# Kernel optimization log

Measured on AMD Instinct MI355X. Metric: run time of the kernel, lower is better.

Reference implementation:

```python
import jax, jax.numpy as jnp
import numpy as np

# SMPL kinematic tree parents (parent index < child index, so a forward loop is valid)
PARENTS = np.array([-1, 0, 0, 0, 1, 2, 3, 4, 5, 6, 7, 8, 9, 9, 9, 12, 13, 14, 16, 17, 18, 19, 20, 21], dtype=np.int32)

B = 131072      # batch
J = 24          # num_joints
D = 6           # dim_per_joint
F = 13 + D      # per-joint MLP width = 19


def setup_inputs() -> dict:
    key = jax.random.key(0)
    ks = jax.random.split(key, 8)
    rots = jax.random.normal(ks[0], (B, J, 9), dtype=jnp.float32)
    Jtrs = jax.random.normal(ks[1], (B, J, 3), dtype=jnp.float32)
    # layer_0: Linear(9*J + 3*J -> D), torch convention W:[out,in]
    W0 = jax.random.normal(ks[2], (D, 12 * J), dtype=jnp.float32) * 0.05
    b0 = jnp.zeros((D,), dtype=jnp.float32)
    # per-joint MLPs, stacked: Linear(F->F), ReLU, Linear(F->D)
    W1 = jax.random.normal(ks[3], (J, F, F), dtype=jnp.float32) * 0.2
    b1 = jnp.zeros((J, F), dtype=jnp.float32)
    W2 = jax.random.normal(ks[4], (J, D, F), dtype=jnp.float32) * 0.2
    b2 = jnp.zeros((J, D), dtype=jnp.float32)
    return {"rots": rots, "Jtrs": Jtrs, "W0": W0, "b0": b0,
            "W1": W1, "b1": b1, "W2": W2, "b2": b2}


def reference(rots, Jtrs, W0, b0, W1, b1, W2, b2):
    bsz = rots.shape[0]
    # global feature: concat flattened rots and Jtrs -> Linear -> [B, D]
    gfeat = jnp.concatenate([rots.reshape(bsz, -1), Jtrs.reshape(bsz, -1)], axis=-1)
    gfeat = gfeat @ W0.T + b0
    out = [None] * J
    for j in range(J):  # fixed small structural loop over kinematic tree
        rot = rots[:, j, :]   # [B, 9]
        jtr = Jtrs[:, j, :]   # [B, 3]
        p = int(PARENTS[j])
        if p == -1:
            bone_l = jnp.linalg.norm(jtr, axis=-1, keepdims=True)  # [B, 1]
            feat = gfeat
        else:
            bone_l = jnp.linalg.norm(jtr - Jtrs[:, p, :], axis=-1, keepdims=True)
            feat = out[p]
        x = jnp.concatenate([rot, jtr, bone_l, feat], axis=-1)     # [B, 19]
        h = jax.nn.relu(x @ W1[j].T + b1[j])
        out[j] = h @ W2[j].T + b2[j]                               # [B, 6]
    return jnp.concatenate(out, axis=-1)  # [B, 144]
```

## Files before the change

kernel.cpp:

```cpp
#include <hip/hip_runtime.h>
#include <math.h>

#define BLK 256

constexpr int PAR_CT[24] = {-1,0,0,0,1,2,3,4,5,6,7,8,9,9,9,12,13,14,16,17,18,19,20,21};

template<int M>
__device__ __forceinline__ float4 bcast_f4(const float4 (&s)[14]) {
    constexpr int lane = M & 3, reg = M >> 2;
    float4 v = s[reg], r;
    r.x = __shfl(v.x, lane, 4);
    r.y = __shfl(v.y, lane, 4);
    r.z = __shfl(v.z, lane, 4);
    r.w = __shfl(v.w, lane, 4);
    return r;
}

template<int E>
__device__ __forceinline__ float bcast_jt(const float4 (&s)[5]) {
    constexpr int m = E >> 2, lane = m & 3, reg = m >> 2, c = E & 3;
    float4 v = s[reg];
    float x = (c == 0) ? v.x : (c == 1) ? v.y : (c == 2) ? v.z : v.w;
    return __shfl(x, lane, 4);
}

template<int J>
__device__ __forceinline__ void joint_step(const float4 (&rot_s)[14],
                                           const float4 (&jt_s)[5],
                                           const float* __restrict__ W1s,
                                           const float* __restrict__ W2s,
                                           const float* __restrict__ b2,
                                           const float (&gf)[6],
                                           float (&o)[24][6],
                                           float* __restrict__ orow,
                                           int l)
{
    constexpr int P = PAR_CT[J];

    const float jx = bcast_jt<3*J+0>(jt_s);
    const float jy = bcast_jt<3*J+1>(jt_s);
    const float jz = bcast_jt<3*J+2>(jt_s);
    float dx, dy, dz;
    if constexpr (P < 0) { dx = jx; dy = jy; dz = jz; }
    else {
        const float px = bcast_jt<3*P+0>(jt_s);
        const float py = bcast_jt<3*P+1>(jt_s);
        const float pz = bcast_jt<3*P+2>(jt_s);
        dx = jx - px; dy = jy - py; dz = jz - pz;
    }
    const float bl = sqrtf(dx*dx + dy*dy + dz*dz);

    constexpr int w0  = (9*J) / 4;
    constexpr int off = (9*J) % 4;
    float4 A = bcast_f4<w0  >(rot_s);
    float4 B = bcast_f4<w0+1>(rot_s);
    float4 C = bcast_f4<w0+2>(rot_s);
    float rv[12] = {A.x,A.y,A.z,A.w, B.x,B.y,B.z,B.w, C.x,C.y,C.z,C.w};

    float f0,f1,f2,f3,f4v,f5;
    if constexpr (P < 0) { f0=gf[0]; f1=gf[1]; f2=gf[2]; f3=gf[3]; f4v=gf[4]; f5=gf[5]; }
    else { f0=o[P][0]; f1=o[P][1]; f2=o[P][2]; f3=o[P][3]; f4v=o[P][4]; f5=o[P][5]; }

    float h[5];
    #pragma unroll
    for (int u = 0; u < 5; ++u) {
        const int r = l + 4*u;
        if (r < 19) {
            const float* w = W1s + J*380 + r*20;
            float4 wa = *(const float4*)(w);
            float4 wb = *(const float4*)(w + 4);
            float4 wc = *(const float4*)(w + 8);
            float4 wd = *(const float4*)(w + 12);
            float4 we = *(const float4*)(w + 16);
            float acc = we.w;
            acc = fmaf(rv[off+0], wa.x, acc);
            acc = fmaf(rv[off+1], wa.y, acc);
            acc = fmaf(rv[off+2], wa.z, acc);
            acc = fmaf(rv[off+3], wa.w, acc);
            acc = fmaf(rv[off+4], wb.x, acc);
            acc = fmaf(rv[off+5], wb.y, acc);
            acc = fmaf(rv[off+6], wb.z, acc);
            acc = fmaf(rv[off+7], wb.w, acc);
            acc = fmaf(rv[off+8], wc.x, acc);
            acc = fmaf(jx, wc.y, acc);
            acc = fmaf(jy, wc.z, acc);
            acc = fmaf(jz, wc.w, acc);
            acc = fmaf(bl, wd.x, acc);
            acc = fmaf(f0, wd.y, acc);
            acc = fmaf(f1, wd.z, acc);
            acc = fmaf(f2, wd.w, acc);
            acc = fmaf(f3, we.x, acc);
            acc = fmaf(f4v, we.y, acc);
            acc = fmaf(f5, we.z, acc);
            h[u] = fmaxf(acc, 0.0f);
        }
    }

    float od[6] = {0,0,0,0,0,0};
    #pragma unroll
    for (int u = 0; u < 5; ++u) {
        const int r = l + 4*u;
        if (r < 19) {
            const float* w = W2s + J*152 + r*8;
            float4 wa = *(const float4*)(w);
            float4 wb = *(const float4*)(w + 4);
            od[0] = fmaf(h[u], wa.x, od[0]);
            od[1] = fmaf(h[u], wa.y, od[1]);
            od[2] = fmaf(h[u], wa.z, od[2]);
            od[3] = fmaf(h[u], wa.w, od[3]);
            od[4] = fmaf(h[u], wb.x, od[4]);
            od[5] = fmaf(h[u], wb.y, od[5]);
        }
    }

    #pragma unroll
    for (int d = 0; d < 6; ++d) {
        od[d] += __shfl_xor(od[d], 1, 4);
        od[d] += __shfl_xor(od[d], 2, 4);
        od[d] += b2[J*6 + d];
        o[J][d] = od[d];
    }

    if constexpr (J & 1) {
        if (l < 3) {
            float4 v;
            if (l == 0)      { v.x = o[J-1][0]; v.y = o[J-1][1]; v.z = o[J-1][2]; v.w = o[J-1][3]; }
            else if (l == 1) { v.x = o[J-1][4]; v.y = o[J-1][5]; v.z = o[J][0];   v.w = o[J][1];   }
            else             { v.x = o[J][2];   v.y = o[J][3];   v.z = o[J][4];   v.w = o[J][5];   }
            *reinterpret_cast<float4*>(orow + (J-1)*6 + 4*l) = v;
        }
    }
}

template<int J>
__device__ __forceinline__ void run_chain(const float4 (&rot_s)[14],
                                          const float4 (&jt_s)[5],
                                          const float* __restrict__ W1s,
                                          const float* __restrict__ W2s,
                                          const float* __restrict__ b2,
                                          const float (&gf)[6],
                                          float (&o)[24][6],
                                          float* __restrict__ orow,
                                          int l)
{
    if constexpr (J < 24) {
        joint_step<J>(rot_s, jt_s, W1s, W2s, b2, gf, o, orow, l);
        run_chain<J+1>(rot_s, jt_s, W1s, W2s, b2, gf, o, orow, l);
    }
}

__global__ __launch_bounds__(BLK, 3)
void pose_kernel(const float* __restrict__ rots,
                 const float* __restrict__ jtrs,
                 const float* __restrict__ W0,
                 const float* __restrict__ b0,
                 const float* __restrict__ W1,
                 const float* __restrict__ b1,
                 const float* __restrict__ W2,
                 const float* __restrict__ b2,
                 float* __restrict__ out,
                 int bsz)
{
    __shared__ __align__(16) float W1s[24*19*20];
    __shared__ __align__(16) float W2s[24*19*8];

    for (int idx = threadIdx.x; idx < 24*19*20; idx += BLK) {
        int j = idx / 380, rem = idx % 380, r = rem / 20, c = rem % 20;
        W1s[idx] = (c < 19) ? W1[(j*19 + r)*19 + c] : b1[j*19 + r];
    }
    for (int idx = threadIdx.x; idx < 24*19*8; idx += BLK) {
        int j = idx / 152, rem = idx % 152, r = rem / 8, d = rem % 8;
        W2s[idx] = (d < 6) ? W2[(j*6 + d)*19 + r] : 0.0f;
    }
    __syncthreads();

    const int t   = blockIdx.x * BLK + threadIdx.x;
    const int row = t >> 2;
    const int l   = t & 3;
    if (row >= bsz) return;

    const float4* rp = reinterpret_cast<const float4*>(rots + (size_t)row * 216);
    const float4* jp = reinterpret_cast<const float4*>(jtrs + (size_t)row * 72);
    float* orow = out + (size_t)row * 144;

    float4 rot_s[14];
    #pragma unroll
    for (int i = 0; i < 13; ++i) rot_s[i] = rp[4*i + l];
    if (l < 2) rot_s[13] = rp[52 + l];

    float4 jt_s[5];
    #pragma unroll
    for (int i = 0; i < 4; ++i) jt_s[i] = jp[4*i + l];
    if (l < 2) jt_s[4] = jp[16 + l];

    float gf[6] = {0,0,0,0,0,0};
    #pragma unroll
    for (int i = 0; i < 13; ++i) {
        const int m = 4*i + l;
        float4 v = rot_s[i];
        #pragma unroll
        for (int d = 0; d < 6; ++d) {
            float4 w = *reinterpret_cast<const float4*>(W0 + d*288 + 4*m);
            gf[d] = fmaf(v.x, w.x, gf[d]);
            gf[d] = fmaf(v.y, w.y, gf[d]);
            gf[d] = fmaf(v.z, w.z, gf[d]);
            gf[d] = fmaf(v.w, w.w, gf[d]);
        }
    }
    if (l < 2) {
        const int m = 52 + l;
        float4 v = rot_s[13];
        #pragma unroll
        for (int d = 0; d < 6; ++d) {
            float4 w = *reinterpret_cast<const float4*>(W0 + d*288 + 4*m);
            gf[d] = fmaf(v.x, w.x, gf[d]);
            gf[d] = fmaf(v.y, w.y, gf[d]);
            gf[d] = fmaf(v.z, w.z, gf[d]);
            gf[d] = fmaf(v.w, w.w, gf[d]);
        }
    }
    #pragma unroll
    for (int i = 0; i < 4; ++i) {
        const int m = 4*i + l;
        float4 v = jt_s[i];
        #pragma unroll
        for (int d = 0; d < 6; ++d) {
            float4 w = *reinterpret_cast<const float4*>(W0 + d*288 + 216 + 4*m);
            gf[d] = fmaf(v.x, w.x, gf[d]);
            gf[d] = fmaf(v.y, w.y, gf[d]);
            gf[d] = fmaf(v.z, w.z, gf[d]);
            gf[d] = fmaf(v.w, w.w, gf[d]);
        }
    }
    if (l < 2) {
        const int m = 16 + l;
        float4 v = jt_s[4];
        #pragma unroll
        for (int d = 0; d < 6; ++d) {
            float4 w = *reinterpret_cast<const float4*>(W0 + d*288 + 216 + 4*m);
            gf[d] = fmaf(v.x, w.x, gf[d]);
            gf[d] = fmaf(v.y, w.y, gf[d]);
            gf[d] = fmaf(v.z, w.z, gf[d]);
            gf[d] = fmaf(v.w, w.w, gf[d]);
        }
    }
    #pragma unroll
    for (int d = 0; d < 6; ++d) {
        gf[d] += __shfl_xor(gf[d], 1, 4);
        gf[d] += __shfl_xor(gf[d], 2, 4);
        gf[d] += b0[d];
    }

    float o[24][6];
    run_chain<0>(rot_s, jt_s, W1s, W2s, b2, gf, o, orow, l);
}

extern "C" void kernel_launch(void* const* d_in, const int* in_sizes, int n_in,
                              void* d_out, int out_size, void* d_ws, size_t ws_size,
                              hipStream_t stream)
{
    const float* rots = (const float*)d_in[0];
    const float* jtrs = (const float*)d_in[1];
    const float* W0   = (const float*)d_in[2];
    const float* b0   = (const float*)d_in[3];
    const float* W1   = (const float*)d_in[4];
    const float* b1   = (const float*)d_in[5];
    const float* W2   = (const float*)d_in[6];
    const float* b2   = (const float*)d_in[7];
    float* out = (float*)d_out;

    int bsz = in_sizes[0] / 216;
    long long threads = (long long)bsz * 4;
    int blocks = (int)((threads + BLK - 1) / BLK);
    hipLaunchKernelGGL(pose_kernel, dim3(blocks), dim3(BLK), 0, stream,
                       rots, jtrs, W0, b0, W1, b1, W2, b2, out, bsz);
}
```

Before: 342.3 us.

## Interleave independent kinematic-tree joints in groups to expose instruction-level parallelism

Replaces the strictly sequential per-joint chain with groups of up to three joints whose parents are already computed, interleaving their layer-1 and layer-2 computations and shuffle reductions. The goal is to hide shuffle and LDS latency along the serial dependency chain by overlapping independent work. This raises register pressure (three sets of rotation, h and od values live at once), which may cause spills under the launch bounds of 3 blocks.

```diff
diff --git a/kernel.cpp b/kernel.cpp
--- a/kernel.cpp
+++ b/kernel.cpp
@@ -24,95 +24,106 @@
     return __shfl(x, lane, 4);
 }
 
-template<int J>
-__device__ __forceinline__ void joint_step(const float4 (&rot_s)[14],
-                                           const float4 (&jt_s)[5],
-                                           const float* __restrict__ W1s,
-                                           const float* __restrict__ W2s,
-                                           const float* __restrict__ b2,
-                                           const float (&gf)[6],
-                                           float (&o)[24][6],
-                                           float* __restrict__ orow,
-                                           int l)
+struct JS {
+    float rv[12];
+    float jx, jy, jz, bl;
+};
+
+template<int J>
+__device__ __forceinline__ void prep(const float4 (&rot_s)[14], const float4 (&jt_s)[5], JS& s)
 {
     constexpr int P = PAR_CT[J];
-
-    const float jx = bcast_jt<3*J+0>(jt_s);
-    const float jy = bcast_jt<3*J+1>(jt_s);
-    const float jz = bcast_jt<3*J+2>(jt_s);
+    s.jx = bcast_jt<3*J+0>(jt_s);
+    s.jy = bcast_jt<3*J+1>(jt_s);
+    s.jz = bcast_jt<3*J+2>(jt_s);
     float dx, dy, dz;
-    if constexpr (P < 0) { dx = jx; dy = jy; dz = jz; }
+    if constexpr (P < 0) { dx = s.jx; dy = s.jy; dz = s.jz; }
     else {
         const float px = bcast_jt<3*P+0>(jt_s);
         const float py = bcast_jt<3*P+1>(jt_s);
         const float pz = bcast_jt<3*P+2>(jt_s);
-        dx = jx - px; dy = jy - py; dz = jz - pz;
-    }
-    const float bl = sqrtf(dx*dx + dy*dy + dz*dz);
-
-    constexpr int w0  = (9*J) / 4;
-    constexpr int off = (9*J) % 4;
+        dx = s.jx - px; dy = s.jy - py; dz = s.jz - pz;
+    }
+    s.bl = sqrtf(dx*dx + dy*dy + dz*dz);
+
+    constexpr int w0 = (9*J) / 4;
     float4 A = bcast_f4<w0  >(rot_s);
     float4 B = bcast_f4<w0+1>(rot_s);
     float4 C = bcast_f4<w0+2>(rot_s);
-    float rv[12] = {A.x,A.y,A.z,A.w, B.x,B.y,B.z,B.w, C.x,C.y,C.z,C.w};
-
-    float f0,f1,f2,f3,f4v,f5;
-    if constexpr (P < 0) { f0=gf[0]; f1=gf[1]; f2=gf[2]; f3=gf[3]; f4v=gf[4]; f5=gf[5]; }
-    else { f0=o[P][0]; f1=o[P][1]; f2=o[P][2]; f3=o[P][3]; f4v=o[P][4]; f5=o[P][5]; }
-
-    float h[5];
-    #pragma unroll
-    for (int u = 0; u < 5; ++u) {
-        const int r = l + 4*u;
-        if (r < 19) {
-            const float* w = W1s + J*380 + r*20;
-            float4 wa = *(const float4*)(w);
-            float4 wb = *(const float4*)(w + 4);
-            float4 wc = *(const float4*)(w + 8);
-            float4 wd = *(const float4*)(w + 12);
-            float4 we = *(const float4*)(w + 16);
-            float acc = we.w;
-            acc = fmaf(rv[off+0], wa.x, acc);
-            acc = fmaf(rv[off+1], wa.y, acc);
-            acc = fmaf(rv[off+2], wa.z, acc);
-            acc = fmaf(rv[off+3], wa.w, acc);
-            acc = fmaf(rv[off+4], wb.x, acc);
-            acc = fmaf(rv[off+5], wb.y, acc);
-            acc = fmaf(rv[off+6], wb.z, acc);
-            acc = fmaf(rv[off+7], wb.w, acc);
-            acc = fmaf(rv[off+8], wc.x, acc);
-            acc = fmaf(jx, wc.y, acc);
-            acc = fmaf(jy, wc.z, acc);
-            acc = fmaf(jz, wc.w, acc);
-            acc = fmaf(bl, wd.x, acc);
-            acc = fmaf(f0, wd.y, acc);
-            acc = fmaf(f1, wd.z, acc);
-            acc = fmaf(f2, wd.w, acc);
-            acc = fmaf(f3, we.x, acc);
-            acc = fmaf(f4v, we.y, acc);
-            acc = fmaf(f5, we.z, acc);
-            h[u] = fmaxf(acc, 0.0f);
-        }
-    }
-
-    float od[6] = {0,0,0,0,0,0};
-    #pragma unroll
-    for (int u = 0; u < 5; ++u) {
-        const int r = l + 4*u;
-        if (r < 19) {
-            const float* w = W2s + J*152 + r*8;
-            float4 wa = *(const float4*)(w);
-            float4 wb = *(const float4*)(w + 4);
-            od[0] = fmaf(h[u], wa.x, od[0]);
-            od[1] = fmaf(h[u], wa.y, od[1]);
-            od[2] = fmaf(h[u], wa.z, od[2]);
-            od[3] = fmaf(h[u], wa.w, od[3]);
-            od[4] = fmaf(h[u], wb.x, od[4]);
-            od[5] = fmaf(h[u], wb.y, od[5]);
-        }
-    }
-
+    s.rv[0]=A.x; s.rv[1]=A.y; s.rv[2]=A.z; s.rv[3]=A.w;
+    s.rv[4]=B.x; s.rv[5]=B.y; s.rv[6]=B.z; s.rv[7]=B.w;
+    s.rv[8]=C.x; s.rv[9]=C.y; s.rv[10]=C.z; s.rv[11]=C.w;
+}
+
+template<int J>
+__device__ __forceinline__ void l1row(const JS& s, const float (&gf)[6], const float (&o)[24][6],
+                                      int u, int l, const float* __restrict__ W1s, float (&h)[5])
+{
+    constexpr int P   = PAR_CT[J];
+    constexpr int off = (9*J) % 4;
+    const int r = l + 4*u;
+    if (r < 19) {
+        const float* w = W1s + J*380 + r*20;
+        float4 wa = *(const float4*)(w);
+        float4 wb = *(const float4*)(w + 4);
+        float4 wc = *(const float4*)(w + 8);
+        float4 wd = *(const float4*)(w + 12);
+        float4 we = *(const float4*)(w + 16);
+        float acc = we.w;
+        acc = fmaf(s.rv[off+0], wa.x, acc);
+        acc = fmaf(s.rv[off+1], wa.y, acc);
+        acc = fmaf(s.rv[off+2], wa.z, acc);
+        acc = fmaf(s.rv[off+3], wa.w, acc);
+        acc = fmaf(s.rv[off+4], wb.x, acc);
+        acc = fmaf(s.rv[off+5], wb.y, acc);
+        acc = fmaf(s.rv[off+6], wb.z, acc);
+        acc = fmaf(s.rv[off+7], wb.w, acc);
+        acc = fmaf(s.rv[off+8], wc.x, acc);
+        acc = fmaf(s.jx, wc.y, acc);
+        acc = fmaf(s.jy, wc.z, acc);
+        acc = fmaf(s.jz, wc.w, acc);
+        acc = fmaf(s.bl, wd.x, acc);
+        if constexpr (P < 0) {
+            acc = fmaf(gf[0], wd.y, acc);
+            acc = fmaf(gf[1], wd.z, acc);
+            acc = fmaf(gf[2], wd.w, acc);
+            acc = fmaf(gf[3], we.x, acc);
+            acc = fmaf(gf[4], we.y, acc);
+            acc = fmaf(gf[5], we.z, acc);
+        } else {
+            acc = fmaf(o[P][0], wd.y, acc);
+            acc = fmaf(o[P][1], wd.z, acc);
+            acc = fmaf(o[P][2], wd.w, acc);
+            acc = fmaf(o[P][3], we.x, acc);
+            acc = fmaf(o[P][4], we.y, acc);
+            acc = fmaf(o[P][5], we.z, acc);
+        }
+        h[u] = fmaxf(acc, 0.0f);
+    }
+}
+
+template<int J>
+__device__ __forceinline__ void l2row(const float (&h)[5], int u, int l,
+                                      const float* __restrict__ W2s, float (&od)[6])
+{
+    const int r = l + 4*u;
+    if (r < 19) {
+        const float* w = W2s + J*152 + r*8;
+        float4 wa = *(const float4*)(w);
+        float4 wb = *(const float4*)(w + 4);
+        od[0] = fmaf(h[u], wa.x, od[0]);
+        od[1] = fmaf(h[u], wa.y, od[1]);
+        od[2] = fmaf(h[u], wa.z, od[2]);
+        od[3] = fmaf(h[u], wa.w, od[3]);
+        od[4] = fmaf(h[u], wb.x, od[4]);
+        od[5] = fmaf(h[u], wb.y, od[5]);
+    }
+}
+
+template<int J>
+__device__ __forceinline__ void finishJ(float (&od)[6], const float* __restrict__ b2,
+                                        float (&o)[24][6])
+{
     #pragma unroll
     for (int d = 0; d < 6; ++d) {
         od[d] += __shfl_xor(od[d], 1, 4);
@@ -120,33 +131,57 @@
         od[d] += b2[J*6 + d];
         o[J][d] = od[d];
     }
-
-    if constexpr (J & 1) {
-        if (l < 3) {
-            float4 v;
-            if (l == 0)      { v.x = o[J-1][0]; v.y = o[J-1][1]; v.z = o[J-1][2]; v.w = o[J-1][3]; }
-            else if (l == 1) { v.x = o[J-1][4]; v.y = o[J-1][5]; v.z = o[J][0];   v.w = o[J][1];   }
-            else             { v.x = o[J][2];   v.y = o[J][3];   v.z = o[J][4];   v.w = o[J][5];   }
-            *reinterpret_cast<float4*>(orow + (J-1)*6 + 4*l) = v;
-        }
-    }
-}
-
-template<int J>
-__device__ __forceinline__ void run_chain(const float4 (&rot_s)[14],
-                                          const float4 (&jt_s)[5],
-                                          const float* __restrict__ W1s,
-                                          const float* __restrict__ W2s,
-                                          const float* __restrict__ b2,
-                                          const float (&gf)[6],
-                                          float (&o)[24][6],
-                                          float* __restrict__ orow,
-                                          int l)
-{
-    if constexpr (J < 24) {
-        joint_step<J>(rot_s, jt_s, W1s, W2s, b2, gf, o, orow, l);
-        run_chain<J+1>(rot_s, jt_s, W1s, W2s, b2, gf, o, orow, l);
-    }
+}
+
+template<int J>
+__device__ __forceinline__ void store_pair(const float (&o)[24][6], float* __restrict__ orow, int l)
+{
+    static_assert(J & 1, "pair store at odd J");
+    if (l < 3) {
+        float4 v;
+        if (l == 0)      { v.x = o[J-1][0]; v.y = o[J-1][1]; v.z = o[J-1][2]; v.w = o[J-1][3]; }
+        else if (l == 1) { v.x = o[J-1][4]; v.y = o[J-1][5]; v.z = o[J][0];   v.w = o[J][1];   }
+        else             { v.x = o[J][2];   v.y = o[J][3];   v.z = o[J][4];   v.w = o[J][5];   }
+        *reinterpret_cast<float4*>(orow + (J-1)*6 + 4*l) = v;
+    }
+}
+
+template<int JA, int JB, int JC>
+__device__ __forceinline__ void group_step(const float4 (&rot_s)[14], const float4 (&jt_s)[5],
+                                           const float* __restrict__ W1s,
+                                           const float* __restrict__ W2s,
+                                           const float* __restrict__ b2,
+                                           const float (&gf)[6], float (&o)[24][6],
+                                           float* __restrict__ orow, int l)
+{
+    JS sA, sB, sC;
+    prep<JA>(rot_s, jt_s, sA);
+    if constexpr (JB >= 0) prep<JB>(rot_s, jt_s, sB);
+    if constexpr (JC >= 0) prep<JC>(rot_s, jt_s, sC);
+
+    float hA[5], hB[5], hC[5];
+    #pragma unroll
+    for (int u = 0; u < 5; ++u) {
+        l1row<JA>(sA, gf, o, u, l, W1s, hA);
+        if constexpr (JB >= 0) l1row<JB>(sB, gf, o, u, l, W1s, hB);
+        if constexpr (JC >= 0) l1row<JC>(sC, gf, o, u, l, W1s, hC);
+    }
+
+    float odA[6] = {0,0,0,0,0,0}, odB[6] = {0,0,0,0,0,0}, odC[6] = {0,0,0,0,0,0};
+    #pragma unroll
+    for (int u = 0; u < 5; ++u) {
+        l2row<JA>(hA, u, l, W2s, odA);
+        if constexpr (JB >= 0) l2row<JB>(hB, u, l, W2s, odB);
+        if constexpr (JC >= 0) l2row<JC>(hC, u, l, W2s, odC);
+    }
+
+    finishJ<JA>(odA, b2, o);
+    if constexpr (JB >= 0) finishJ<JB>(odB, b2, o);
+    if constexpr (JC >= 0) finishJ<JC>(odC, b2, o);
+
+    if constexpr (JA & 1) store_pair<JA>(o, orow, l);
+    if constexpr (JB >= 0) { if constexpr (JB & 1) store_pair<JB>(o, orow, l); }
+    if constexpr (JC >= 0) { if constexpr (JC & 1) store_pair<JC>(o, orow, l); }
 }
 
 __global__ __launch_bounds__(BLK, 3)
@@ -252,7 +287,16 @@
     }
 
     float o[24][6];
-    run_chain<0>(rot_s, jt_s, W1s, W2s, b2, gf, o, orow, l);
+    group_step< 0,-1,-1>(rot_s, jt_s, W1s, W2s, b2, gf, o, orow, l);
+    group_step< 1, 2, 3>(rot_s, jt_s, W1s, W2s, b2, gf, o, orow, l);
+    group_step< 4, 5, 6>(rot_s, jt_s, W1s, W2s, b2, gf, o, orow, l);
+    group_step< 7, 8, 9>(rot_s, jt_s, W1s, W2s, b2, gf, o, orow, l);
+    group_step<10,11,12>(rot_s, jt_s, W1s, W2s, b2, gf, o, orow, l);
+    group_step<13,14,-1>(rot_s, jt_s, W1s, W2s, b2, gf, o, orow, l);
+    group_step<15,16,17>(rot_s, jt_s, W1s, W2s, b2, gf, o, orow, l);
+    group_step<18,19,-1>(rot_s, jt_s, W1s, W2s, b2, gf, o, orow, l);
+    group_step<20,21,-1>(rot_s, jt_s, W1s, W2s, b2, gf, o, orow, l);
+    group_step<22,23,-1>(rot_s, jt_s, W1s, W2s, b2, gf, o, orow, l);
 }
 
 extern "C" void kernel_launch(void* const* d_in, const int* in_sizes, int n_in,
```

Measured after the change: 744.2 us. 2.17x slower.
